# Optimization experiments

Hardware: AMD Instinct MI355X
Metric: run time of the kernel (lower is better)

The kernel has to match this reference:

```python
import jax, jax.numpy as jnp
import numpy as np

FEATURE_SIZE = 10 * 64 * 64  # 40960
HIDDEN1 = 512
HIDDEN2 = 256
BATCH = 4096


def setup_inputs() -> dict:
    key = jax.random.key(0)
    ks = jax.random.split(key, 8)
    # Sparse binary-ish features emulated as dense uniform (math is identical).
    white_features = jax.random.uniform(ks[0], (BATCH, FEATURE_SIZE), dtype=jnp.float32)
    black_features = jax.random.uniform(ks[1], (BATCH, FEATURE_SIZE), dtype=jnp.float32)
    s_ft = 1.0 / np.sqrt(FEATURE_SIZE)
    s_fc1 = 1.0 / np.sqrt(HIDDEN1 * 2)
    s_fc2 = 1.0 / np.sqrt(HIDDEN2)
    ft_w = jax.random.uniform(ks[2], (HIDDEN1, FEATURE_SIZE), minval=-s_ft, maxval=s_ft, dtype=jnp.float32)
    ft_b = jax.random.uniform(ks[3], (HIDDEN1,), minval=-s_ft, maxval=s_ft, dtype=jnp.float32)
    fc1_w = jax.random.uniform(ks[4], (HIDDEN2, HIDDEN1 * 2), minval=-s_fc1, maxval=s_fc1, dtype=jnp.float32)
    fc1_b = jax.random.uniform(ks[5], (HIDDEN2,), minval=-s_fc1, maxval=s_fc1, dtype=jnp.float32)
    fc2_w = jax.random.uniform(ks[6], (1, HIDDEN2), minval=-s_fc2, maxval=s_fc2, dtype=jnp.float32)
    fc2_b = jax.random.uniform(ks[7], (1,), minval=-s_fc2, maxval=s_fc2, dtype=jnp.float32)
    return dict(white_features=white_features, black_features=black_features,
                ft_w=ft_w, ft_b=ft_b, fc1_w=fc1_w, fc1_b=fc1_b, fc2_w=fc2_w, fc2_b=fc2_b)


def reference(white_features, black_features, ft_w, ft_b, fc1_w, fc1_b, fc2_w, fc2_b):
    # Feature transform per perspective, clamped to [0, 1]
    white_ft = jnp.clip(white_features @ ft_w.T + ft_b, 0.0, 1.0)  # [B, H1]
    black_ft = jnp.clip(black_features @ ft_w.T + ft_b, 0.0, 1.0)  # [B, H1]
    combined = jnp.concatenate([white_ft, black_ft], axis=1)       # [B, 2*H1]
    x = jax.nn.relu(combined @ fc1_w.T + fc1_b)                    # [B, H2]
    x = x @ fc2_w.T + fc2_b                                        # [B, 1]
    return x.squeeze(-1)
```

## Files before the change

### kernel.cpp

```cpp
#include <hip/hip_runtime.h>
#include <stdint.h>

#define BATCH 4096
#define FEAT  40960
#define H1    512
#define KS    4
#define KCHUNK (FEAT / KS)
#define NSTEPS (KCHUNK / 32)
#define NTILES (FEAT / 32)
#define WTILE  32768

typedef float f32x4 __attribute__((ext_vector_type(4)));
typedef short s16x8 __attribute__((ext_vector_type(8)));
typedef unsigned int u32x2 __attribute__((ext_vector_type(2)));
typedef unsigned int u32x4 __attribute__((ext_vector_type(4)));

__device__ __forceinline__ unsigned bfpack2(float lo, float hi) {
  unsigned a = __float_as_uint(lo);
  unsigned b = __float_as_uint(hi);
  a += 0x7FFFu + ((a >> 16) & 1u);
  b += 0x7FFFu + ((b >> 16) & 1u);
  return (a >> 16) | (b & 0xFFFF0000u);
}

__device__ __forceinline__ int lds_swz(int r, int cb) {
  return (r << 6) + (cb ^ (((r >> 1) & 3) << 4));
}

__device__ __forceinline__ void glds16(const void* g, void* l) {
  __builtin_amdgcn_global_load_lds(
      (const __attribute__((address_space(1))) unsigned*)g,
      (__attribute__((address_space(3))) unsigned*)l, 16, 0, 0);
}

__global__ __launch_bounds__(512)
void wcvt_kernel(const float* __restrict__ ftw, char* __restrict__ wbf) {
  const int bid = blockIdx.x;
  const int T = bid >> 2, rq = bid & 3;
  const int tid = threadIdx.x;
  const int r = rq * 128 + (tid >> 2), kq = tid & 3;
  const float* src = ftw + (size_t)r * FEAT + T * 32 + kq * 8;
  f32x4 v0 = *(const f32x4*)src;
  f32x4 v1 = *(const f32x4*)(src + 4);
  u32x4 o;
  o.x = bfpack2(v0.x, v0.y); o.y = bfpack2(v0.z, v0.w);
  o.z = bfpack2(v1.x, v1.y); o.w = bfpack2(v1.z, v1.w);
  *(u32x4*)(wbf + (size_t)T * WTILE + lds_swz(r, kq * 16)) = o;
}

__global__ __launch_bounds__(512, 2)
void ft_gemm_kernel(const float* __restrict__ whiteF,
                    const float* __restrict__ blackF,
                    const char* __restrict__ wbf,
                    float* __restrict__ Ppart) {
  __shared__ char smem[81920];

  const int tid = threadIdx.x, bid = blockIdx.x;
  const int ks = bid >> 6;
  const int p  = bid & 1;
  const int mt = (bid >> 1) & 31;

  const float* Ag =
      (p == 0 ? whiteF : blackF) + (size_t)(mt * 128) * FEAT + ks * KCHUNK;

  const int a_row = tid >> 2, a_kq = tid & 3;
  const float* aptr = Ag + (size_t)a_row * FEAT + a_kq * 8;
  const int awoff = lds_swz(a_row, a_kq * 16);

  const int lane = tid & 63, wave = tid >> 6;
  const char* wsrc = wbf + (size_t)(ks * NSTEPS) * WTILE + wave * 4096 + lane * 16;
  const int wdst = 8192 + wave * 4096;

  const int wm = wave >> 2, wn = wave & 3;
  const int lrow = lane & 15, lkb = (lane >> 4) * 16;
  int a_off[4], b_off[8];
#pragma unroll
  for (int m = 0; m < 4; ++m) a_off[m] = lds_swz(wm * 64 + m * 16 + lrow, lkb);
#pragma unroll
  for (int n = 0; n < 8; ++n) b_off[n] = 8192 + lds_swz(wn * 128 + n * 16 + lrow, lkb);

  f32x4 acc[4][8];
#pragma unroll
  for (int m = 0; m < 4; ++m)
#pragma unroll
    for (int n = 0; n < 8; ++n) acc[m][n] = (f32x4){0.f, 0.f, 0.f, 0.f};

  f32x4 raA[2], raB[2];

#pragma unroll
  for (int c = 0; c < 4; ++c) glds16(wsrc + c * 1024, smem + wdst + c * 1024);
  raA[0] = *(const f32x4*)aptr;
  raB[0] = *(const f32x4*)(aptr + 4);

#define GSTEP(B, LAST, t)                                                     \
  {                                                                           \
    if (!(LAST)) {                                                            \
      const float* ap = aptr + (size_t)((t) + 1) * 32;                        \
      raA[(B) ^ 1] = *(const f32x4*)ap;                                       \
      raB[(B) ^ 1] = *(const f32x4*)(ap + 4);                                 \
    }                                                                         \
    u32x4 av;                                                                 \
    av.x = bfpack2(raA[B].x, raA[B].y); av.y = bfpack2(raA[B].z, raA[B].w);   \
    av.z = bfpack2(raB[B].x, raB[B].y); av.w = bfpack2(raB[B].z, raB[B].w);   \
    *(u32x4*)(smem + (B) * 40960 + awoff) = av;                               \
    __builtin_amdgcn_sched_barrier(0);                                        \
    if (LAST) { asm volatile("s_waitcnt vmcnt(0) lgkmcnt(0)" ::: "memory"); } \
    else      { asm volatile("s_waitcnt vmcnt(2) lgkmcnt(0)" ::: "memory"); } \
    __builtin_amdgcn_sched_barrier(0);                                        \
    __builtin_amdgcn_s_barrier();                                             \
    __builtin_amdgcn_sched_barrier(0);                                        \
    const char* base = smem + (B) * 40960;                                    \
    s16x8 af[4];                                                              \
    _Pragma("unroll") for (int m = 0; m < 4; ++m)                             \
        af[m] = *(const s16x8*)(base + a_off[m]);                             \
    s16x8 bfr[8];                                                             \
    _Pragma("unroll") for (int n = 0; n < 8; ++n)                             \
        bfr[n] = *(const s16x8*)(base + b_off[n]);                            \
    if (!(LAST)) {                                                            \
      const char* wsp = wsrc + (size_t)((t) + 1) * WTILE;                     \
      char* wdp = smem + ((B) ^ 1) * 40960 + wdst;                            \
      _Pragma("unroll") for (int c = 0; c < 4; ++c)                           \
          glds16(wsp + c * 1024, wdp + c * 1024);                             \
    }                                                                         \
    _Pragma("unroll") for (int n = 0; n < 8; ++n)                             \
      _Pragma("unroll") for (int m = 0; m < 4; ++m)                           \
          acc[m][n] = __builtin_amdgcn_mfma_f32_16x16x32_bf16(                \
              af[m], bfr[n], acc[m][n], 0, 0, 0);                             \
  }

  for (int tt = 0; tt < NSTEPS - 2; tt += 2) {
    GSTEP(0, false, tt);
    GSTEP(1, false, tt + 1);
  }
  GSTEP(0, false, NSTEPS - 2);
  GSTEP(1, true, NSTEPS - 1);
#undef GSTEP

  float* Pp = Ppart + ((size_t)(ks * 2 + p) * BATCH + mt * 128) * H1;
  const int r0 = wm * 64 + (lane >> 4) * 4;
  const int c0 = wn * 128 + lrow;
#pragma unroll
  for (int m = 0; m < 4; ++m)
#pragma unroll
    for (int n = 0; n < 8; ++n) {
      float* dst = Pp + (size_t)(r0 + m * 16) * H1 + c0 + n * 16;
#pragma unroll
      for (int j = 0; j < 4; ++j) dst[(size_t)j * H1] = acc[m][n][j];
    }
}

__global__ __launch_bounds__(256)
void ft_reduce_kernel(const float* __restrict__ Ppart,
                      const float* __restrict__ ftb,
                      unsigned short* __restrict__ comb) {
  const size_t gid = (size_t)blockIdx.x * 256 + threadIdx.x;
  const int    pp  = (int)(gid / (BATCH * H1 / 4));
  const size_t rem = gid % (BATCH * H1 / 4);
  const int    row = (int)(rem / (H1 / 4));
  const int    n4  = (int)(rem % (H1 / 4)) * 4;

  f32x4 s = (f32x4){0.f, 0.f, 0.f, 0.f};
#pragma unroll
  for (int ks = 0; ks < KS; ++ks)
    s += *(const f32x4*)(Ppart + ((size_t)(ks * 2 + pp) * BATCH + row) * H1 + n4);
  const f32x4 bv = *(const f32x4*)(ftb + n4);
  s += bv;
  s.x = fminf(fmaxf(s.x, 0.f), 1.f);
  s.y = fminf(fmaxf(s.y, 0.f), 1.f);
  s.z = fminf(fmaxf(s.z, 0.f), 1.f);
  s.w = fminf(fmaxf(s.w, 0.f), 1.f);

  u32x2 o;
  o.x = bfpack2(s.x, s.y);
  o.y = bfpack2(s.z, s.w);
  *(u32x2*)(comb + (size_t)row * 1024 + pp * H1 + n4) = o;
}

__global__ __launch_bounds__(256)
void fc_kernel(const unsigned short* __restrict__ comb,
               const float* __restrict__ w1, const float* __restrict__ b1,
               const float* __restrict__ w2, const float* __restrict__ b2,
               float* __restrict__ out) {
  __shared__ char smem[40960];
  __shared__ float rowsum[64];

  const int tid = threadIdx.x;
  const int bm  = blockIdx.x;
  if (tid < 64) rowsum[tid] = 0.f;

  const int a_row = tid >> 2, a_kq = tid & 3;
  const unsigned short* aptr = comb + (size_t)(bm * 64 + a_row) * 1024 + a_kq * 8;
  const float* wptr = w1 + (size_t)a_row * 1024 + a_kq * 8;

  u32x4 raA;
  f32x4 rw0[4], rw1[4];
  auto issue = [&](int t) {
    raA = *(const u32x4*)(aptr + t * 32);
    const float* wp = wptr + t * 32;
#pragma unroll
    for (int s = 0; s < 4; ++s) {
      rw0[s] = *(const f32x4*)(wp + (size_t)s * 64 * 1024);
      rw1[s] = *(const f32x4*)(wp + (size_t)s * 64 * 1024 + 4);
    }
  };

  const int aoff_w = lds_swz(a_row, a_kq * 16);
  int woff_w[4];
#pragma unroll
  for (int s = 0; s < 4; ++s)
    woff_w[s] = 4096 + lds_swz(s * 64 + a_row, a_kq * 16);

  auto cvtwrite = [&](int b) {
    char* base = smem + b * 20480;
    *(u32x4*)(base + aoff_w) = raA;
#pragma unroll
    for (int s = 0; s < 4; ++s) {
      u32x4 wv;
      wv.x = bfpack2(rw0[s].x, rw0[s].y); wv.y = bfpack2(rw0[s].z, rw0[s].w);
      wv.z = bfpack2(rw1[s].x, rw1[s].y); wv.w = bfpack2(rw1[s].z, rw1[s].w);
      *(u32x4*)(base + woff_w[s]) = wv;
    }
  };

  const int lane = tid & 63, wn = tid >> 6;
  const int lrow = lane & 15, lkb = (lane >> 4) * 16;
  int a_off[4], b_off[4];
#pragma unroll
  for (int m = 0; m < 4; ++m) a_off[m] = lds_swz(m * 16 + lrow, lkb);
#pragma unroll
  for (int n = 0; n < 4; ++n) b_off[n] = 4096 + lds_swz(wn * 64 + n * 16 + lrow, lkb);

  f32x4 acc[4][4];
#pragma unroll
  for (int m = 0; m < 4; ++m)
#pragma unroll
    for (int n = 0; n < 4; ++n) acc[m][n] = (f32x4){0.f, 0.f, 0.f, 0.f};

  issue(0);
  for (int t = 0; t < 32; ++t) {
    const int b = t & 1;
    cvtwrite(b);
    if (t + 1 < 32) issue(t + 1);
    asm volatile("s_waitcnt lgkmcnt(0)" ::: "memory");
    __builtin_amdgcn_sched_barrier(0);
    __builtin_amdgcn_s_barrier();
    __builtin_amdgcn_sched_barrier(0);
    char* base = smem + b * 20480;
    s16x8 af[4];
#pragma unroll
    for (int m = 0; m < 4; ++m) af[m] = *(const s16x8*)(base + a_off[m]);
#pragma unroll
    for (int n = 0; n < 4; ++n) {
      s16x8 bfn = *(const s16x8*)(base + b_off[n]);
#pragma unroll
      for (int m = 0; m < 4; ++m)
        acc[m][n] = __builtin_amdgcn_mfma_f32_16x16x32_bf16(af[m], bfn, acc[m][n], 0, 0, 0);
    }
  }

  float b1v[4], w2v[4];
#pragma unroll
  for (int n = 0; n < 4; ++n) {
    const int col = wn * 64 + n * 16 + lrow;
    b1v[n] = b1[col];
    w2v[n] = w2[col];
  }
#pragma unroll
  for (int m = 0; m < 4; ++m)
#pragma unroll
    for (int j = 0; j < 4; ++j) {
      float v = 0.f;
#pragma unroll
      for (int n = 0; n < 4; ++n) {
        float x = acc[m][n][j] + b1v[n];
        x = fmaxf(x, 0.f);
        v += x * w2v[n];
      }
#pragma unroll
      for (int d = 1; d < 16; d <<= 1) v += __shfl_xor(v, d, 64);
      if ((lane & 15) == 0)
        atomicAdd(&rowsum[m * 16 + (lane >> 4) * 4 + j], v);
    }
  __syncthreads();
  if (tid < 64) {
    out[bm * 64 + tid] = rowsum[tid] + b2[0];
  }
}

extern "C" void kernel_launch(void* const* d_in, const int* in_sizes, int n_in,
                              void* d_out, int out_size, void* d_ws, size_t ws_size,
                              hipStream_t stream) {
  const float* whiteF = (const float*)d_in[0];
  const float* blackF = (const float*)d_in[1];
  const float* ftw    = (const float*)d_in[2];
  const float* ftb    = (const float*)d_in[3];
  const float* w1     = (const float*)d_in[4];
  const float* b1     = (const float*)d_in[5];
  const float* w2     = (const float*)d_in[6];
  const float* b2     = (const float*)d_in[7];

  char* wbf = (char*)d_ws;
  const size_t wbf_bytes   = (size_t)NTILES * WTILE;
  const size_t ppart_bytes = (size_t)KS * 2 * BATCH * H1 * sizeof(float);
  float* Ppart = (float*)((char*)d_ws + wbf_bytes);
  unsigned short* comb = (unsigned short*)((char*)d_ws + wbf_bytes + ppart_bytes);
  float* outp = (float*)d_out;

  hipLaunchKernelGGL(wcvt_kernel, dim3(NTILES * 4), dim3(512), 0, stream, ftw, wbf);
  hipLaunchKernelGGL(ft_gemm_kernel, dim3(64 * KS), dim3(512), 0, stream,
                     whiteF, blackF, wbf, Ppart);
  hipLaunchKernelGGL(ft_reduce_kernel, dim3((2 * BATCH * H1 / 4) / 256), dim3(256),
                     0, stream, Ppart, ftb, comb);
  hipLaunchKernelGGL(fc_kernel, dim3(BATCH / 64), dim3(256), 0, stream,
                     comb, w1, b1, w2, b2, outp);
}
```

Measured before the change: 584.6 us.

## Shrink FT GEMM M-tile to 64 rows, double grid, remap blocks across XCDs

The feature-transform GEMM tile changes from 128x512 to 64x512, so the grid grows from 256 to 512 workgroups and LDS per block drops. Occupancy is raised to 4 blocks per CU, and block IDs are remapped so consecutive IDs spread across the 8 XCDs and neighbouring tiles share the L2. B fragments are now loaded per n-iteration to cut register pressure. The aim is to fill all CUs and hide load latency, at the cost of loading the bf16 weight tile twice as often per output row.

```diff
diff --git a/kernel.cpp b/kernel.cpp
--- a/kernel.cpp
+++ b/kernel.cpp
@@ -9,6 +9,8 @@
 #define NSTEPS (KCHUNK / 32)
 #define NTILES (FEAT / 32)
 #define WTILE  32768
+#define BUFSTRIDE 36864
+#define ALDS 32768
 
 typedef float f32x4 __attribute__((ext_vector_type(4)));
 typedef short s16x8 __attribute__((ext_vector_type(8)));
@@ -48,84 +50,79 @@
   *(u32x4*)(wbf + (size_t)T * WTILE + lds_swz(r, kq * 16)) = o;
 }
 
-__global__ __launch_bounds__(512, 2)
+__global__ __launch_bounds__(512, 4)
 void ft_gemm_kernel(const float* __restrict__ whiteF,
                     const float* __restrict__ blackF,
                     const char* __restrict__ wbf,
                     float* __restrict__ Ppart) {
-  __shared__ char smem[81920];
+  __shared__ char smem[2 * BUFSTRIDE];
 
   const int tid = threadIdx.x, bid = blockIdx.x;
-  const int ks = bid >> 6;
-  const int p  = bid & 1;
-  const int mt = (bid >> 1) & 31;
+  const int wgid = (bid & 7) * 64 + (bid >> 3);
+  const int ks = wgid >> 7;
+  const int p  = (wgid >> 6) & 1;
+  const int mt = wgid & 63;
 
   const float* Ag =
-      (p == 0 ? whiteF : blackF) + (size_t)(mt * 128) * FEAT + ks * KCHUNK;
-
-  const int a_row = tid >> 2, a_kq = tid & 3;
-  const float* aptr = Ag + (size_t)a_row * FEAT + a_kq * 8;
-  const int awoff = lds_swz(a_row, a_kq * 16);
+      (p == 0 ? whiteF : blackF) + (size_t)(mt * 64) * FEAT + ks * KCHUNK;
+
+  const int a_row = tid >> 3, a_kq = tid & 7;
+  const float* aptr = Ag + (size_t)a_row * FEAT + a_kq * 4;
+  const int awoff = ALDS + lds_swz(a_row, a_kq * 8);
 
   const int lane = tid & 63, wave = tid >> 6;
-  const char* wsrc = wbf + (size_t)(ks * NSTEPS) * WTILE + wave * 4096 + lane * 16;
-  const int wdst = 8192 + wave * 4096;
-
-  const int wm = wave >> 2, wn = wave & 3;
+  const char* wsrc = wbf + (size_t)ks * NSTEPS * WTILE + wave * 4096 + lane * 16;
+  const int wdst = wave * 4096;
+
+  const int wn = wave;
   const int lrow = lane & 15, lkb = (lane >> 4) * 16;
-  int a_off[4], b_off[8];
-#pragma unroll
-  for (int m = 0; m < 4; ++m) a_off[m] = lds_swz(wm * 64 + m * 16 + lrow, lkb);
-#pragma unroll
-  for (int n = 0; n < 8; ++n) b_off[n] = 8192 + lds_swz(wn * 128 + n * 16 + lrow, lkb);
-
-  f32x4 acc[4][8];
+  int a_off[4], b_off[4];
+#pragma unroll
+  for (int m = 0; m < 4; ++m) a_off[m] = ALDS + lds_swz(m * 16 + lrow, lkb);
+#pragma unroll
+  for (int n = 0; n < 4; ++n) b_off[n] = lds_swz(wn * 64 + n * 16 + lrow, lkb);
+
+  f32x4 acc[4][4];
 #pragma unroll
   for (int m = 0; m < 4; ++m)
 #pragma unroll
-    for (int n = 0; n < 8; ++n) acc[m][n] = (f32x4){0.f, 0.f, 0.f, 0.f};
-
-  f32x4 raA[2], raB[2];
+    for (int n = 0; n < 4; ++n) acc[m][n] = (f32x4){0.f, 0.f, 0.f, 0.f};
+
+  f32x4 raA[2];
 
 #pragma unroll
   for (int c = 0; c < 4; ++c) glds16(wsrc + c * 1024, smem + wdst + c * 1024);
   raA[0] = *(const f32x4*)aptr;
-  raB[0] = *(const f32x4*)(aptr + 4);
 
 #define GSTEP(B, LAST, t)                                                     \
   {                                                                           \
-    if (!(LAST)) {                                                            \
-      const float* ap = aptr + (size_t)((t) + 1) * 32;                        \
-      raA[(B) ^ 1] = *(const f32x4*)ap;                                       \
-      raB[(B) ^ 1] = *(const f32x4*)(ap + 4);                                 \
-    }                                                                         \
-    u32x4 av;                                                                 \
-    av.x = bfpack2(raA[B].x, raA[B].y); av.y = bfpack2(raA[B].z, raA[B].w);   \
-    av.z = bfpack2(raB[B].x, raB[B].y); av.w = bfpack2(raB[B].z, raB[B].w);   \
-    *(u32x4*)(smem + (B) * 40960 + awoff) = av;                               \
+    if (!(LAST)) raA[(B) ^ 1] = *(const f32x4*)(aptr + (size_t)((t) + 1) * 32); \
+    u32x2 av;                                                                 \
+    av.x = bfpack2(raA[B].x, raA[B].y);                                       \
+    av.y = bfpack2(raA[B].z, raA[B].w);                                       \
+    *(u32x2*)(smem + (B) * BUFSTRIDE + awoff) = av;                           \
     __builtin_amdgcn_sched_barrier(0);                                        \
     if (LAST) { asm volatile("s_waitcnt vmcnt(0) lgkmcnt(0)" ::: "memory"); } \
-    else      { asm volatile("s_waitcnt vmcnt(2) lgkmcnt(0)" ::: "memory"); } \
+    else      { asm volatile("s_waitcnt vmcnt(1) lgkmcnt(0)" ::: "memory"); } \
     __builtin_amdgcn_sched_barrier(0);                                        \
     __builtin_amdgcn_s_barrier();                                             \
     __builtin_amdgcn_sched_barrier(0);                                        \
-    const char* base = smem + (B) * 40960;                                    \
+    const char* base = smem + (B) * BUFSTRIDE;                                \
     s16x8 af[4];                                                              \
     _Pragma("unroll") for (int m = 0; m < 4; ++m)                             \
         af[m] = *(const s16x8*)(base + a_off[m]);                             \
-    s16x8 bfr[8];                                                             \
-    _Pragma("unroll") for (int n = 0; n < 8; ++n)                             \
-        bfr[n] = *(const s16x8*)(base + b_off[n]);                            \
     if (!(LAST)) {                                                            \
       const char* wsp = wsrc + (size_t)((t) + 1) * WTILE;                     \
-      char* wdp = smem + ((B) ^ 1) * 40960 + wdst;                            \
+      char* wdp = smem + ((B) ^ 1) * BUFSTRIDE + wdst;                        \
       _Pragma("unroll") for (int c = 0; c < 4; ++c)                           \
           glds16(wsp + c * 1024, wdp + c * 1024);                             \
     }                                                                         \
-    _Pragma("unroll") for (int n = 0; n < 8; ++n)                             \
+    _Pragma("unroll") for (int n = 0; n < 4; ++n) {                           \
+      s16x8 bfn = *(const s16x8*)(base + b_off[n]);                           \
       _Pragma("unroll") for (int m = 0; m < 4; ++m)                           \
           acc[m][n] = __builtin_amdgcn_mfma_f32_16x16x32_bf16(                \
-              af[m], bfr[n], acc[m][n], 0, 0, 0);                             \
+              af[m], bfn, acc[m][n], 0, 0, 0);                                \
+    }                                                                         \
   }
 
   for (int tt = 0; tt < NSTEPS - 2; tt += 2) {
@@ -136,13 +133,13 @@
   GSTEP(1, true, NSTEPS - 1);
 #undef GSTEP
 
-  float* Pp = Ppart + ((size_t)(ks * 2 + p) * BATCH + mt * 128) * H1;
-  const int r0 = wm * 64 + (lane >> 4) * 4;
-  const int c0 = wn * 128 + lrow;
+  float* Pp = Ppart + ((size_t)(ks * 2 + p) * BATCH + mt * 64) * H1;
+  const int r0 = (lane >> 4) * 4;
+  const int c0 = wn * 64 + lrow;
 #pragma unroll
   for (int m = 0; m < 4; ++m)
 #pragma unroll
-    for (int n = 0; n < 8; ++n) {
+    for (int n = 0; n < 4; ++n) {
       float* dst = Pp + (size_t)(r0 + m * 16) * H1 + c0 + n * 16;
 #pragma unroll
       for (int j = 0; j < 4; ++j) dst[(size_t)j * H1] = acc[m][n][j];
@@ -307,7 +304,7 @@
   float* outp = (float*)d_out;
 
   hipLaunchKernelGGL(wcvt_kernel, dim3(NTILES * 4), dim3(512), 0, stream, ftw, wbf);
-  hipLaunchKernelGGL(ft_gemm_kernel, dim3(64 * KS), dim3(512), 0, stream,
+  hipLaunchKernelGGL(ft_gemm_kernel, dim3(512), dim3(512), 0, stream,
                      whiteF, blackF, wbf, Ppart);
   hipLaunchKernelGGL(ft_reduce_kernel, dim3((2 * BATCH * H1 / 4) / 256), dim3(256),
                      0, stream, Ppart, ftb, comb);
```

After: 548.8 us. 6.1% less time.
